# Kernel tuning notes

Measured on AMD Instinct MI355X. Metric: run time of the kernel, lower is better.

Reference implementation:

```python
import jax, jax.numpy as jnp
import numpy as np

B, Q, PAST, MAXC = 2, 1024, 1024, 4096
H, HKV, D, HID = 32, 8, 128, 4096
HALF = D // 2
GROUPS = H // HKV
EPS = 1e-6
SCALE = 1.0 / (D ** 0.5)


def setup_inputs() -> dict:
    key = jax.random.key(0)
    ks = jax.random.split(key, 6)
    hidden_states = jax.random.normal(ks[0], (B, Q, HID), jnp.float32)
    k_cache = jax.random.normal(ks[1], (B, HKV, MAXC, D), jnp.float32)
    v_cache = jax.random.normal(ks[2], (B, HKV, MAXC, D), jnp.float32)
    # rope table: [1, max_pos, head_dim], cos in first half, sin in second half
    inv_freq = 1.0 / (10000.0 ** (jnp.arange(0, HALF, dtype=jnp.float32) / HALF))
    ang = jnp.arange(MAXC, dtype=jnp.float32)[:, None] * inv_freq[None, :]
    rope_rotary_cos_sin = jnp.concatenate([jnp.cos(ang), jnp.sin(ang)], axis=-1)[None]
    context_lengths = jnp.full((B,), Q, dtype=jnp.int32)
    kvcache_start_index = jnp.full((B,), PAST, dtype=jnp.int32)
    w_qkv = jax.random.normal(ks[3], (HID, (H + 2 * HKV) * D), jnp.float32) * 0.02
    w_o = jax.random.normal(ks[4], (HKV * D, HID), jnp.float32) * 0.02
    q_norm_w = jnp.ones((D,), jnp.float32)
    k_norm_w = jnp.ones((D,), jnp.float32)
    return dict(hidden_states=hidden_states, k_cache=k_cache, v_cache=v_cache,
                rope_rotary_cos_sin=rope_rotary_cos_sin,
                context_lengths=context_lengths,
                kvcache_start_index=kvcache_start_index,
                w_qkv=w_qkv, w_o=w_o, q_norm_w=q_norm_w, k_norm_w=k_norm_w)


def _rms_norm(x, w):
    # x: [..., D]; per-head RMSNorm as in EdgeLLMQKNorm
    var = jnp.mean(x * x, axis=-1, keepdims=True)
    return x * jax.lax.rsqrt(var + EPS) * w


def _apply_rope(x, cos, sin):
    # x: [B, h, Q, D]; cos/sin: [B, Q, HALF] gathered by position_ids
    c = cos[:, None, :, :]
    s = sin[:, None, :, :]
    x1, x2 = x[..., :HALF], x[..., HALF:]
    return jnp.concatenate([x1 * c - x2 * s, x2 * c + x1 * s], axis=-1)


def _cache_update(cache, new, pos_ids):
    # cache: [B, HKV, MAXC, D]; new: [B, HKV, Q, D]; pos_ids: [B, Q]
    b_idx = jnp.arange(B)[:, None]  # [B,1]
    cache_t = jnp.swapaxes(cache, 1, 2)          # [B, MAXC, HKV, D]
    new_t = jnp.swapaxes(new, 1, 2)              # [B, Q, HKV, D]
    cache_t = cache_t.at[b_idx, pos_ids].set(new_t)
    return jnp.swapaxes(cache_t, 1, 2)


def reference(hidden_states, k_cache, v_cache, rope_rotary_cos_sin,
              context_lengths, kvcache_start_index, w_qkv, w_o,
              q_norm_w, k_norm_w):
    bsz, q_len, _ = hidden_states.shape
    # fused QKV projection
    qkv = jnp.einsum('bqh,hd->bqd', hidden_states, w_qkv)
    q, k, v = jnp.split(qkv, [H * D, (H + HKV) * D], axis=-1)
    # per-head QK norm (norm_shape = [B, Q, -1, head_dim])
    q = _rms_norm(q.reshape(bsz, q_len, H, D), q_norm_w)
    k = _rms_norm(k.reshape(bsz, q_len, HKV, D), k_norm_w)
    v = v.reshape(bsz, q_len, HKV, D)
    q = jnp.swapaxes(q, 1, 2)   # [B, H, Q, D]
    k = jnp.swapaxes(k, 1, 2)   # [B, HKV, Q, D]
    v = jnp.swapaxes(v, 1, 2)
    # rope tables (batch row 0), gather by position ids
    cos_t = rope_rotary_cos_sin[0, :, :HALF]  # [max_pos, HALF]
    sin_t = rope_rotary_cos_sin[0, :, HALF:]
    pos_ids = kvcache_start_index[:, None] + jnp.arange(q_len, dtype=jnp.int32)[None, :]  # [B,Q]
    cos = cos_t[pos_ids]
    sin = sin_t[pos_ids]
    q = _apply_rope(q, cos, sin)
    k = _apply_rope(k, cos, sin)
    # dynamic KV-cache write at kvcache_start_index
    present_k_cache = _cache_update(k_cache, k, pos_ids)
    present_v_cache = _cache_update(v_cache, v, pos_ids)
    present_length = PAST + Q  # = max(start) + max(context_lengths), static here
    k_present = present_k_cache[:, :, :present_length, :]
    v_present = present_v_cache[:, :, :present_length, :]
    # GQA head expansion
    k_exp = jnp.repeat(k_present, GROUPS, axis=1)   # [B, H, K, D]
    v_exp = jnp.repeat(v_present, GROUPS, axis=1)
    scores = jnp.einsum('bhqd,bhkd->bhqk', q * SCALE, k_exp)
    seq_k = present_length
    offset = seq_k - q_len
    causal = (jnp.arange(seq_k)[None, :] > (jnp.arange(q_len)[:, None] + offset))
    scores = jnp.where(causal[None, None], -jnp.inf, scores)
    attn = jax.nn.softmax(scores, axis=-1)
    out = jnp.einsum('bhqk,bhkd->bhqd', attn, v_exp)  # [B, H, Q, D]
    # norm is None & H > HKV: sum over GQA group dim (faithful to source)
    out = out.reshape(bsz, HKV, GROUPS, q_len, D).sum(axis=2)  # [B, HKV, Q, D]
    out = jnp.swapaxes(out, 1, 2).reshape(bsz, q_len, HKV * D)
    attn_output = jnp.einsum('bqd,dh->bqh', out, w_o)  # [B, Q, HID]
    return attn_output, present_k_cache, present_v_cache
```

## Files before the change

kernel.cpp:

```cpp
#include <hip/hip_runtime.h>


typedef __bf16 bf16;
typedef __attribute__((ext_vector_type(8))) __bf16 bf16x8;
typedef __attribute__((ext_vector_type(4))) __bf16 bf16x4;
typedef __attribute__((ext_vector_type(4))) float f32x4;
typedef __attribute__((ext_vector_type(4))) unsigned int u32x4;

#define NB 2
#define NQ 1024
#define PAST 1024
#define MAXC 4096
#define NH 32
#define NKV 8
#define HD 128
#define HID 4096
#define SEQK 2048
#define QKV_N 6144
#define SCALE 0.08838834764831845f
#define LOG2E 1.4426950408889634f
#define QSCALE (0.08838834764831845f * 1.4426950408889634f)

__device__ __forceinline__ void async16(const bf16* g, bf16* l) {
    __builtin_amdgcn_global_load_lds(
        (const __attribute__((address_space(1))) void*)g,
        (__attribute__((address_space(3))) void*)l, 16, 0, 0);
}

template <bool F32OUT>
__global__ __launch_bounds__(256) void gemm_bb(const bf16* __restrict__ A,
                                               const bf16* __restrict__ Bt,
                                               void* __restrict__ Cv,
                                               int M, int N, int K, int nbx) {
    __shared__ bf16 As[128 * 64];
    __shared__ bf16 Bs[128 * 64];
    const int nwg  = gridDim.x;
    const int cpx  = nwg >> 3;
    const int orig = blockIdx.x;
    const int wg   = (orig & 7) * cpx + (orig >> 3);
    const int by = wg / nbx, bx = wg - by * nbx;
    const int rowBase = by * 128, colBase = bx * 128;

    const int tid  = threadIdx.x;
    const int lane = tid & 63;
    const int wv   = tid >> 6;
    const int wm   = wv >> 1, wn = wv & 1;
    const int l15  = lane & 15, quad = lane >> 4;

    const int sr = lane >> 3;
    const int sc = ((lane & 7) ^ sr) * 8;
    const bf16* aG = A  + (long)(rowBase + wv * 32 + sr) * K + sc;
    const bf16* bG = Bt + (long)(colBase + wv * 32 + sr) * K + sc;
    bf16* aL = &As[(wv * 32) * 64];
    bf16* bL = &Bs[(wv * 32) * 64];

    f32x4 acc[4][4];
#pragma unroll
    for (int i = 0; i < 4; i++)
#pragma unroll
        for (int j = 0; j < 4; j++) acc[i][j] = (f32x4){0.f, 0.f, 0.f, 0.f};

    for (int k0 = 0; k0 < K; k0 += 64) {
#pragma unroll
        for (int j = 0; j < 4; j++) {
            async16(aG + (long)(j * 8) * K + k0, aL + j * 8 * 64);
            async16(bG + (long)(j * 8) * K + k0, bL + j * 8 * 64);
        }
        __syncthreads();
#pragma unroll
        for (int kc = 0; kc < 2; kc++) {
            bf16x8 af[4], bfr[4];
#pragma unroll
            for (int mi = 0; mi < 4; mi++)
                af[mi] = *(const bf16x8*)&As[(wm * 64 + mi * 16 + l15) * 64 +
                                             ((kc * 32 + quad * 8) ^ ((l15 & 7) * 8))];
#pragma unroll
            for (int ni = 0; ni < 4; ni++)
                bfr[ni] = *(const bf16x8*)&Bs[(wn * 64 + ni * 16 + l15) * 64 +
                                              ((kc * 32 + quad * 8) ^ ((l15 & 7) * 8))];
#pragma unroll
            for (int mi = 0; mi < 4; mi++)
#pragma unroll
                for (int ni = 0; ni < 4; ni++)
                    acc[mi][ni] = __builtin_amdgcn_mfma_f32_16x16x32_bf16(
                        af[mi], bfr[ni], acc[mi][ni], 0, 0, 0);
        }
        __syncthreads();
    }
#pragma unroll
    for (int mi = 0; mi < 4; mi++)
#pragma unroll
        for (int r = 0; r < 4; r++) {
            const int row = rowBase + wm * 64 + mi * 16 + quad * 4 + r;
#pragma unroll
            for (int ni = 0; ni < 4; ni++) {
                const int col = colBase + wn * 64 + ni * 16 + l15;
                if (F32OUT) ((float*)Cv)[(long)row * N + col] = acc[mi][ni][r];
                else        ((bf16*)Cv)[(long)row * N + col] = (bf16)acc[mi][ni][r];
            }
        }
}

__global__ void conv_f2b(const float* __restrict__ in, bf16* __restrict__ out) {
    const long e = ((long)blockIdx.x * 256 + threadIdx.x) * 8;
    const f32x4 a = *(const f32x4*)&in[e];
    const f32x4 b = *(const f32x4*)&in[e + 4];
    bf16x8 v;
#pragma unroll
    for (int j = 0; j < 4; j++) { v[j] = (bf16)a[j]; v[4 + j] = (bf16)b[j]; }
    *(bf16x8*)&out[e] = v;
}

__global__ __launch_bounds__(256) void transpose_f2b(const float* __restrict__ in,
                                                     bf16* __restrict__ out,
                                                     int R, int C) {
    __shared__ bf16 t[64][72];
    const int r0 = blockIdx.y * 64, c0 = blockIdx.x * 64;
    const int tid = threadIdx.x;
    const int lr = tid >> 3;
    const int lc = (tid & 7) * 8;
#pragma unroll
    for (int i = 0; i < 2; i++) {
        const f32x4* p = (const f32x4*)&in[(long)(r0 + lr + i * 32) * C + c0 + lc];
        const f32x4 v0 = p[0], v1 = p[1];
        bf16x8 v;
#pragma unroll
        for (int j = 0; j < 4; j++) { v[j] = (bf16)v0[j]; v[4 + j] = (bf16)v1[j]; }
        *(bf16x8*)&t[lr + i * 32][lc] = v;
    }
    __syncthreads();
#pragma unroll
    for (int i = 0; i < 2; i++) {
        const int oc = lr + i * 32;
        bf16x8 v;
#pragma unroll
        for (int j = 0; j < 8; j++) v[j] = t[lc + j][oc];
        *(bf16x8*)&out[(long)(c0 + oc) * R + r0 + lc] = v;
    }
}

__global__ __launch_bounds__(256) void transpose_bf16(const bf16* __restrict__ in,
                                                      bf16* __restrict__ out,
                                                      int R, int C,
                                                      long inBS, long outBS) {
    __shared__ bf16 t[64][72];
    in  += (long)blockIdx.z * inBS;
    out += (long)blockIdx.z * outBS;
    const int r0 = blockIdx.y * 64, c0 = blockIdx.x * 64;
    const int tid = threadIdx.x;
    const int lr = tid >> 3;
    const int lc = (tid & 7) * 8;
#pragma unroll
    for (int i = 0; i < 2; i++)
        *(u32x4*)&t[lr + i * 32][lc] =
            *(const u32x4*)&in[(long)(r0 + lr + i * 32) * C + c0 + lc];
    __syncthreads();
#pragma unroll
    for (int i = 0; i < 2; i++) {
        const int oc = lr + i * 32;
        bf16x8 v;
#pragma unroll
        for (int j = 0; j < 8; j++) v[j] = t[lc + j][oc];
        *(bf16x8*)&out[(long)(c0 + oc) * R + r0 + lc] = v;
    }
}

__global__ void cache_to_bf16(const float* __restrict__ kc, const float* __restrict__ vc,
                              bf16* __restrict__ kb, bf16* __restrict__ vb) {
    const int bh = blockIdx.y;
    const long idx = ((long)blockIdx.x * 256 + threadIdx.x) * 8;
    const float* src = (blockIdx.z ? vc : kc) + (long)bh * MAXC * HD + idx;
    bf16* dst = (blockIdx.z ? vb : kb) + (long)bh * SEQK * HD + idx;
    const f32x4 a = *(const f32x4*)src;
    const f32x4 b = *(const f32x4*)(src + 4);
    bf16x8 v;
#pragma unroll
    for (int j = 0; j < 4; j++) { v[j] = (bf16)a[j]; v[4 + j] = (bf16)b[j]; }
    *(bf16x8*)dst = v;
}

__global__ void qkv_post(const bf16* __restrict__ qkv, const float* __restrict__ cs,
                         const int* __restrict__ kvstart,
                         const float* __restrict__ qw, const float* __restrict__ kw,
                         bf16* __restrict__ qbuf, float* __restrict__ outk,
                         float* __restrict__ outv, bf16* __restrict__ kb,
                         bf16* __restrict__ vb) {
    const int h = blockIdx.x;
    const int q = blockIdx.y;
    const int b = blockIdx.z;
    const int l = threadIdx.x;
    const bf16* x = qkv + (long)(b * NQ + q) * QKV_N + h * HD;
    float x1 = (float)x[l], x2 = (float)x[l + 64];
    const int pos = kvstart[b] + q;
    if (h < 40) {
        float sq = x1 * x1 + x2 * x2;
#pragma unroll
        for (int m = 32; m >= 1; m >>= 1) sq += __shfl_xor(sq, m);
        const float rr = rsqrtf(sq * (1.0f / 128.0f) + 1e-6f);
        const float w1 = (h < 32) ? qw[l] : kw[l];
        const float w2 = (h < 32) ? qw[l + 64] : kw[l + 64];
        const float y1 = x1 * rr * w1;
        const float y2 = x2 * rr * w2;
        const float c = cs[(long)pos * HD + l];
        const float s = cs[(long)pos * HD + 64 + l];
        const float o1 = y1 * c - y2 * s;
        const float o2 = y2 * c + y1 * s;
        if (h < 32) {
            bf16* dst = qbuf + ((long)(b * NH + h) * NQ + q) * HD;
            dst[l] = (bf16)(o1 * QSCALE);
            dst[l + 64] = (bf16)(o2 * QSCALE);
        } else {
            const int hk = h - 32;
            float* df = outk + ((long)(b * NKV + hk) * MAXC + pos) * HD;
            df[l] = o1; df[l + 64] = o2;
            bf16* db = kb + ((long)(b * NKV + hk) * SEQK + pos) * HD;
            db[l] = (bf16)o1; db[l + 64] = (bf16)o2;
        }
    } else {
        const int hk = h - 40;
        float* df = outv + ((long)(b * NKV + hk) * MAXC + pos) * HD;
        df[l] = x1; df[l + 64] = x2;
        bf16* db = vb + ((long)(b * NKV + hk) * SEQK + pos) * HD;
        db[l] = (bf16)x1; db[l + 64] = (bf16)x2;
    }
}

__global__ __launch_bounds__(256, 2) void attn_fwd(const bf16* __restrict__ qbuf,
                                                   const bf16* __restrict__ kb,
                                                   const bf16* __restrict__ vt,
                                                   bf16* __restrict__ oheads) {
    const int ib  = blockIdx.x + 8 * (blockIdx.y + 32 * blockIdx.z);
    const int xc  = ib & 7, j = ib >> 3;
    const int g   = xc * 8 + (j & 7);
    const int h   = g & 31, b = g >> 5;
    const int qraw = j >> 3;
    const int qt  = (qraw < 4) ? qraw : 11 - qraw;
    const int hk  = h >> 2;
    const int tid = threadIdx.x;
    const int lane = tid & 63, wv = tid >> 6;
    const int l15 = lane & 15, quad = lane >> 4;

    __shared__ bf16 Ks[2][64][128];
    __shared__ bf16 Vs[2][128][64];
    __shared__ bf16 Ps[4][32][64];

    const int qb = qt * 128 + wv * 32;

    bf16x8 aq[2][4];
#pragma unroll
    for (int ss = 0; ss < 2; ss++) {
        const bf16* qp = qbuf + ((long)(b * NH + h) * NQ + qb + ss * 16 + l15) * HD + quad * 8;
#pragma unroll
        for (int kc = 0; kc < 4; kc++) aq[ss][kc] = *(const bf16x8*)(qp + kc * 32);
    }

    f32x4 o[2][8];
    float m_[2], l_[2];
#pragma unroll
    for (int ss = 0; ss < 2; ss++) {
#pragma unroll
        for (int dt = 0; dt < 8; dt++) o[ss][dt] = (f32x4){0.f, 0.f, 0.f, 0.f};
        m_[ss] = -1e30f; l_[ss] = 0.f;
    }

    const long kcb = (long)(b * NKV + hk) * SEQK * HD;
    const long vtb = (long)(b * NKV + hk) * HD * (long)SEQK;
    const int ntiles = (qt * 128 + 127 + PAST + 64) >> 6;

    u32x4 kreg[4], vreg[4];
#pragma unroll
    for (int i = 0; i < 4; i++) {
        const int c = tid + i * 256;
        kreg[i] = *(const u32x4*)&kb[kcb + (long)(c >> 4) * HD + (c & 15) * 8];
        vreg[i] = *(const u32x4*)&vt[vtb + (long)(c >> 3) * SEQK + (c & 7) * 8];
    }
#pragma unroll
    for (int i = 0; i < 4; i++) {
        const int c = tid + i * 256;
        const int kr = c >> 4, kc8 = (c & 15) * 8;
        *(u32x4*)&Ks[0][kr][kc8 ^ ((kr & 7) * 8)] = kreg[i];
        const int vr = c >> 3, vc8 = (c & 7) * 8;
        *(u32x4*)&Vs[0][vr][vc8 ^ ((vr & 7) * 8)] = vreg[i];
    }
#pragma unroll
    for (int i = 0; i < 4; i++) {
        const int c = tid + i * 256;
        kreg[i] = *(const u32x4*)&kb[kcb + (long)(64 + (c >> 4)) * HD + (c & 15) * 8];
        vreg[i] = *(const u32x4*)&vt[vtb + (long)(c >> 3) * SEQK + 64 + (c & 7) * 8];
    }
    __syncthreads();

    for (int t = 0; t < ntiles; t++) {
        const int cur = t & 1;
        const int k0 = t * 64;
        if (t + 1 < ntiles) {
#pragma unroll
            for (int i = 0; i < 4; i++) {
                const int c = tid + i * 256;
                const int kr = c >> 4, kc8 = (c & 15) * 8;
                *(u32x4*)&Ks[cur ^ 1][kr][kc8 ^ ((kr & 7) * 8)] = kreg[i];
                const int vr = c >> 3, vc8 = (c & 7) * 8;
                *(u32x4*)&Vs[cur ^ 1][vr][vc8 ^ ((vr & 7) * 8)] = vreg[i];
            }
        }
        if (t + 2 < ntiles) {
            const int k0n = k0 + 128;
#pragma unroll
            for (int i = 0; i < 4; i++) {
                const int c = tid + i * 256;
                kreg[i] = *(const u32x4*)&kb[kcb + (long)(k0n + (c >> 4)) * HD + (c & 15) * 8];
                vreg[i] = *(const u32x4*)&vt[vtb + (long)(c >> 3) * SEQK + k0n + (c & 7) * 8];
            }
        }

#pragma unroll
        for (int ss = 0; ss < 2; ss++) {
            const int rbase = qb + ss * 16;
            if (k0 > rbase + 15 + PAST) continue;
            f32x4 s[4];
#pragma unroll
            for (int nk = 0; nk < 4; nk++) s[nk] = (f32x4){0.f, 0.f, 0.f, 0.f};
            __builtin_amdgcn_s_setprio(1);
#pragma unroll
            for (int kc = 0; kc < 4; kc++)
#pragma unroll
                for (int nk = 0; nk < 4; nk++) {
                    const bf16x8 bk = *(const bf16x8*)
                        &Ks[cur][nk * 16 + l15][(kc * 32 + quad * 8) ^ ((l15 & 7) * 8)];
                    s[nk] = __builtin_amdgcn_mfma_f32_16x16x32_bf16(bk, aq[ss][kc], s[nk], 0, 0, 0);
                }
            __builtin_amdgcn_s_setprio(0);
            if (k0 + 63 > rbase + PAST) {
                const int lim = rbase + l15 + PAST - k0;
#pragma unroll
                for (int nk = 0; nk < 4; nk++)
#pragma unroll
                    for (int r = 0; r < 4; r++)
                        if (nk * 16 + quad * 4 + r > lim) s[nk][r] = -1e30f;
            }
            float mx = s[0][0];
#pragma unroll
            for (int nk = 0; nk < 4; nk++)
#pragma unroll
                for (int r = 0; r < 4; r++) mx = fmaxf(mx, s[nk][r]);
            mx = fmaxf(mx, __shfl_xor(mx, 16));
            mx = fmaxf(mx, __shfl_xor(mx, 32));
            const float mn = fmaxf(m_[ss], mx);
            const float alpha = exp2f(m_[ss] - mn);
            float sum = 0.f;
#pragma unroll
            for (int nk = 0; nk < 4; nk++)
#pragma unroll
                for (int r = 0; r < 4; r++) {
                    const float p = exp2f(s[nk][r] - mn);
                    s[nk][r] = p;
                    sum += p;
                }
            sum += __shfl_xor(sum, 16);
            sum += __shfl_xor(sum, 32);
            l_[ss] = l_[ss] * alpha + sum;
            m_[ss] = mn;
#pragma unroll
            for (int nk = 0; nk < 4; nk++) {
                bf16x4 pv;
#pragma unroll
                for (int r = 0; r < 4; r++) pv[r] = (bf16)s[nk][r];
                *(bf16x4*)&Ps[wv][ss * 16 + l15][(nk * 16 + quad * 4) ^ ((l15 & 7) * 8)] = pv;
            }
#pragma unroll
            for (int r = 0; r < 4; r++) {
                const float ar = __shfl(alpha, (lane & 48) + quad * 4 + r);
#pragma unroll
                for (int dt = 0; dt < 8; dt++) o[ss][dt][r] *= ar;
            }
        }
#pragma unroll
        for (int ss = 0; ss < 2; ss++) {
            const int rbase = qb + ss * 16;
            if (k0 > rbase + 15 + PAST) continue;
            __builtin_amdgcn_s_setprio(1);
#pragma unroll
            for (int kc = 0; kc < 2; kc++) {
                const bf16x8 ap = *(const bf16x8*)
                    &Ps[wv][ss * 16 + l15][(kc * 32 + quad * 8) ^ ((l15 & 7) * 8)];
#pragma unroll
                for (int dt = 0; dt < 8; dt++) {
                    const bf16x8 bv = *(const bf16x8*)
                        &Vs[cur][dt * 16 + l15][(kc * 32 + quad * 8) ^ ((l15 & 7) * 8)];
                    o[ss][dt] = __builtin_amdgcn_mfma_f32_16x16x32_bf16(ap, bv, o[ss][dt], 0, 0, 0);
                }
            }
            __builtin_amdgcn_s_setprio(0);
        }
        __syncthreads();
    }

#pragma unroll
    for (int ss = 0; ss < 2; ss++) {
        float inv[4];
#pragma unroll
        for (int r = 0; r < 4; r++) {
            const float lr = __shfl(l_[ss], (lane & 48) + quad * 4 + r);
            inv[r] = 1.0f / lr;
        }
#pragma unroll
        for (int dt = 0; dt < 8; dt++)
#pragma unroll
            for (int r = 0; r < 4; r++) {
                const int row = qb + ss * 16 + quad * 4 + r;
                oheads[((long)(b * NH + h) * NQ + row) * HD + dt * 16 + l15] =
                    (bf16)(o[ss][dt][r] * inv[r]);
            }
    }
}

__global__ void group_sum(const bf16* __restrict__ oheads, bf16* __restrict__ osum) {
    const long e = ((long)blockIdx.x * 256 + threadIdx.x) * 8;
    const int b = (int)(e >> 20);
    const int rem = (int)(e & 1048575);
    const int q = rem >> 10;
    const int col = rem & 1023;
    const int hk = col >> 7;
    const int d = col & 127;
    float acc[8] = {0.f, 0.f, 0.f, 0.f, 0.f, 0.f, 0.f, 0.f};
#pragma unroll
    for (int g = 0; g < 4; g++) {
        const bf16x8 v = *(const bf16x8*)
            &oheads[((long)(b * NH + hk * 4 + g) * NQ + q) * HD + d];
#pragma unroll
        for (int j = 0; j < 8; j++) acc[j] += (float)v[j];
    }
    bf16x8 r;
#pragma unroll
    for (int j = 0; j < 8; j++) r[j] = (bf16)acc[j];
    *(bf16x8*)&osum[e] = r;
}

extern "C" void kernel_launch(void* const* d_in, const int* in_sizes, int n_in,
                              void* d_out, int out_size, void* d_ws, size_t ws_size,
                              hipStream_t stream) {
    const float* hidden  = (const float*)d_in[0];
    const float* kc_in   = (const float*)d_in[1];
    const float* vc_in   = (const float*)d_in[2];
    const float* rope_cs = (const float*)d_in[3];
    const int*   kvstart = (const int*)d_in[5];
    const float* w_qkv   = (const float*)d_in[6];
    const float* w_o     = (const float*)d_in[7];
    const float* qnw     = (const float*)d_in[8];
    const float* knw     = (const float*)d_in[9];

    float* out_attn = (float*)d_out;
    float* out_k    = out_attn + 8388608L;
    float* out_v    = out_k + 8388608L;

    char* ob = (char*)d_out;
    bf16* qbuf  = (bf16*)ob;
    bf16* kb16  = (bf16*)(ob + 16777216);
    bf16* vtb16 = (bf16*)(ob + 25165824);
    bf16* wqkvT = (bf16*)(ob + 33554432);
    bf16* hb16  = (bf16*)(ob + 83886080);

    char* ws = (char*)d_ws;
    bf16*  qkvb   = (bf16*)ws;
    bf16*  vpb16  = (bf16*)(ws + 25165824);
    bf16*  oheads = (bf16*)ws;
    bf16*  osum   = (bf16*)(ws + 16777216);
    bf16*  woT    = (bf16*)(ws + 25165824);

    conv_f2b<<<dim3(4096), 256, 0, stream>>>(hidden, hb16);
    transpose_f2b<<<dim3(96, 64), 256, 0, stream>>>(w_qkv, wqkvT, HID, QKV_N);
    gemm_bb<false><<<dim3(768), 256, 0, stream>>>(hb16, wqkvT, qkvb, 2048, QKV_N, HID, 48);
    hipMemcpyAsync(out_k, kc_in, 33554432, hipMemcpyDeviceToDevice, stream);
    hipMemcpyAsync(out_v, vc_in, 33554432, hipMemcpyDeviceToDevice, stream);
    cache_to_bf16<<<dim3(128, 16, 2), 256, 0, stream>>>(kc_in, vc_in, kb16, vpb16);
    qkv_post<<<dim3(48, NQ, NB), 64, 0, stream>>>(qkvb, rope_cs, kvstart, qnw, knw,
                                                  qbuf, out_k, out_v, kb16, vpb16);
    transpose_bf16<<<dim3(2, 32, 16), 256, 0, stream>>>(vpb16, vtb16, SEQK, HD,
                                                        (long)SEQK * HD, (long)SEQK * HD);
    attn_fwd<<<dim3(8, NH, NB), 256, 0, stream>>>(qbuf, kb16, vtb16, oheads);
    group_sum<<<dim3(1024), 256, 0, stream>>>(oheads, osum);
    transpose_f2b<<<dim3(64, 16), 256, 0, stream>>>(w_o, woT, 1024, HID);
    gemm_bb<true><<<dim3(512), 256, 0, stream>>>(osum, woT, out_attn, 2048, HID, 1024, 32);
}
```

Baseline: 581.9 us.

## Use 256x256 double-buffered GEMM for QKV projection and pipeline loads

Adds a 256x256-tile, 512-thread GEMM kernel with double-buffered LDS and async prefetch of the next K tile, used for the QKV projection. The existing 128x128 GEMM (still used for the output projection) also gets double buffering, and both raise wave priority around the MFMA block. The goal is more operand reuse per tile and overlap of global loads with matrix math. The cost is doubled LDS (128KB per block for gemm256) and higher register pressure, and the QKV grid shrinks to 192 workgroups, which may underfill the CUs.

```diff
diff --git a/kernel.cpp b/kernel.cpp
--- a/kernel.cpp
+++ b/kernel.cpp
@@ -28,12 +28,97 @@
 }
 
 template <bool F32OUT>
+__global__ __launch_bounds__(512, 2) void gemm256(const bf16* __restrict__ A,
+                                                  const bf16* __restrict__ Bt,
+                                                  void* __restrict__ Cv,
+                                                  int N, int K) {
+    __shared__ bf16 As[2][256 * 64];
+    __shared__ bf16 Bs[2][256 * 64];
+    const int nwg  = gridDim.x;
+    const int cpx  = nwg >> 3;
+    const int orig = blockIdx.x;
+    const int wg   = (orig & 7) * cpx + (orig >> 3);
+    const int by   = wg & 7, bx = wg >> 3;
+    const int rowBase = by * 256, colBase = bx * 256;
+
+    const int tid  = threadIdx.x;
+    const int lane = tid & 63;
+    const int wv   = tid >> 6;
+    const int wm   = wv >> 2, wn = wv & 3;
+    const int l15  = lane & 15, quad = lane >> 4;
+
+    const int sr = lane >> 3;
+    const int sc = ((lane & 7) ^ sr) * 8;
+    const bf16* aG = A  + (long)(rowBase + wv * 32 + sr) * K + sc;
+    const bf16* bG = Bt + (long)(colBase + wv * 32 + sr) * K + sc;
+
+    f32x4 acc[8][4];
+#pragma unroll
+    for (int i = 0; i < 8; i++)
+#pragma unroll
+        for (int j = 0; j < 4; j++) acc[i][j] = (f32x4){0.f, 0.f, 0.f, 0.f};
+
+    const int nt = K >> 6;
+#pragma unroll
+    for (int j = 0; j < 4; j++) {
+        async16(aG + (long)(j * 8) * K, &As[0][(wv * 32 + j * 8) * 64]);
+        async16(bG + (long)(j * 8) * K, &Bs[0][(wv * 32 + j * 8) * 64]);
+    }
+    __syncthreads();
+
+    for (int t = 0; t < nt; t++) {
+        const int cur = t & 1;
+        if (t + 1 < nt) {
+            const int kn = (t + 1) << 6;
+#pragma unroll
+            for (int j = 0; j < 4; j++) {
+                async16(aG + (long)(j * 8) * K + kn, &As[cur ^ 1][(wv * 32 + j * 8) * 64]);
+                async16(bG + (long)(j * 8) * K + kn, &Bs[cur ^ 1][(wv * 32 + j * 8) * 64]);
+            }
+        }
+#pragma unroll
+        for (int kc = 0; kc < 2; kc++) {
+            bf16x8 af[8], bfr[4];
+#pragma unroll
+            for (int mi = 0; mi < 8; mi++)
+                af[mi] = *(const bf16x8*)&As[cur][(wm * 128 + mi * 16 + l15) * 64 +
+                                                  ((kc * 32 + quad * 8) ^ ((l15 & 7) * 8))];
+#pragma unroll
+            for (int ni = 0; ni < 4; ni++)
+                bfr[ni] = *(const bf16x8*)&Bs[cur][(wn * 64 + ni * 16 + l15) * 64 +
+                                                   ((kc * 32 + quad * 8) ^ ((l15 & 7) * 8))];
+            __builtin_amdgcn_s_setprio(1);
+#pragma unroll
+            for (int mi = 0; mi < 8; mi++)
+#pragma unroll
+                for (int ni = 0; ni < 4; ni++)
+                    acc[mi][ni] = __builtin_amdgcn_mfma_f32_16x16x32_bf16(
+                        af[mi], bfr[ni], acc[mi][ni], 0, 0, 0);
+            __builtin_amdgcn_s_setprio(0);
+        }
+        __syncthreads();
+    }
+#pragma unroll
+    for (int mi = 0; mi < 8; mi++)
+#pragma unroll
+        for (int r = 0; r < 4; r++) {
+            const int row = rowBase + wm * 128 + mi * 16 + quad * 4 + r;
+#pragma unroll
+            for (int ni = 0; ni < 4; ni++) {
+                const int col = colBase + wn * 64 + ni * 16 + l15;
+                if (F32OUT) ((float*)Cv)[(long)row * N + col] = acc[mi][ni][r];
+                else        ((bf16*)Cv)[(long)row * N + col] = (bf16)acc[mi][ni][r];
+            }
+        }
+}
+
+template <bool F32OUT>
 __global__ __launch_bounds__(256) void gemm_bb(const bf16* __restrict__ A,
                                                const bf16* __restrict__ Bt,
                                                void* __restrict__ Cv,
                                                int M, int N, int K, int nbx) {
-    __shared__ bf16 As[128 * 64];
-    __shared__ bf16 Bs[128 * 64];
+    __shared__ bf16 As[2][128 * 64];
+    __shared__ bf16 Bs[2][128 * 64];
     const int nwg  = gridDim.x;
     const int cpx  = nwg >> 3;
     const int orig = blockIdx.x;
@@ -51,8 +136,6 @@
     const int sc = ((lane & 7) ^ sr) * 8;
     const bf16* aG = A  + (long)(rowBase + wv * 32 + sr) * K + sc;
     const bf16* bG = Bt + (long)(colBase + wv * 32 + sr) * K + sc;
-    bf16* aL = &As[(wv * 32) * 64];
-    bf16* bL = &Bs[(wv * 32) * 64];
 
     f32x4 acc[4][4];
 #pragma unroll
@@ -60,30 +143,43 @@
 #pragma unroll
         for (int j = 0; j < 4; j++) acc[i][j] = (f32x4){0.f, 0.f, 0.f, 0.f};
 
-    for (int k0 = 0; k0 < K; k0 += 64) {
-#pragma unroll
-        for (int j = 0; j < 4; j++) {
-            async16(aG + (long)(j * 8) * K + k0, aL + j * 8 * 64);
-            async16(bG + (long)(j * 8) * K + k0, bL + j * 8 * 64);
-        }
-        __syncthreads();
+    const int nt = K >> 6;
+#pragma unroll
+    for (int j = 0; j < 4; j++) {
+        async16(aG + (long)(j * 8) * K, &As[0][(wv * 32 + j * 8) * 64]);
+        async16(bG + (long)(j * 8) * K, &Bs[0][(wv * 32 + j * 8) * 64]);
+    }
+    __syncthreads();
+
+    for (int t = 0; t < nt; t++) {
+        const int cur = t & 1;
+        if (t + 1 < nt) {
+            const int kn = (t + 1) << 6;
+#pragma unroll
+            for (int j = 0; j < 4; j++) {
+                async16(aG + (long)(j * 8) * K + kn, &As[cur ^ 1][(wv * 32 + j * 8) * 64]);
+                async16(bG + (long)(j * 8) * K + kn, &Bs[cur ^ 1][(wv * 32 + j * 8) * 64]);
+            }
+        }
 #pragma unroll
         for (int kc = 0; kc < 2; kc++) {
             bf16x8 af[4], bfr[4];
 #pragma unroll
             for (int mi = 0; mi < 4; mi++)
-                af[mi] = *(const bf16x8*)&As[(wm * 64 + mi * 16 + l15) * 64 +
-                                             ((kc * 32 + quad * 8) ^ ((l15 & 7) * 8))];
+                af[mi] = *(const bf16x8*)&As[cur][(wm * 64 + mi * 16 + l15) * 64 +
+                                                  ((kc * 32 + quad * 8) ^ ((l15 & 7) * 8))];
 #pragma unroll
             for (int ni = 0; ni < 4; ni++)
-                bfr[ni] = *(const bf16x8*)&Bs[(wn * 64 + ni * 16 + l15) * 64 +
-                                              ((kc * 32 + quad * 8) ^ ((l15 & 7) * 8))];
+                bfr[ni] = *(const bf16x8*)&Bs[cur][(wn * 64 + ni * 16 + l15) * 64 +
+                                                   ((kc * 32 + quad * 8) ^ ((l15 & 7) * 8))];
+            __builtin_amdgcn_s_setprio(1);
 #pragma unroll
             for (int mi = 0; mi < 4; mi++)
 #pragma unroll
                 for (int ni = 0; ni < 4; ni++)
                     acc[mi][ni] = __builtin_amdgcn_mfma_f32_16x16x32_bf16(
                         af[mi], bfr[ni], acc[mi][ni], 0, 0, 0);
+            __builtin_amdgcn_s_setprio(0);
         }
         __syncthreads();
     }
@@ -469,7 +565,7 @@
 
     conv_f2b<<<dim3(4096), 256, 0, stream>>>(hidden, hb16);
     transpose_f2b<<<dim3(96, 64), 256, 0, stream>>>(w_qkv, wqkvT, HID, QKV_N);
-    gemm_bb<false><<<dim3(768), 256, 0, stream>>>(hb16, wqkvT, qkvb, 2048, QKV_N, HID, 48);
+    gemm256<false><<<dim3(192), 512, 0, stream>>>(hb16, wqkvT, qkvb, QKV_N, HID);
     hipMemcpyAsync(out_k, kc_in, 33554432, hipMemcpyDeviceToDevice, stream);
     hipMemcpyAsync(out_v, vc_in, 33554432, hipMemcpyDeviceToDevice, stream);
     cache_to_bf16<<<dim3(128, 16, 2), 256, 0, stream>>>(kc_in, vc_in, kb16, vpb16);
```

Result: faster. 568.4 us (-2.3%).
